# Kernel optimization log

Hardware: AMD Instinct MI355X
Metric: run time of the kernel (lower is better)

The kernel has to match this reference:

```python
import jax, jax.numpy as jnp
import numpy as np

N_NODES = 50000
N_EDGES = 800000
T_STEPS = 12
IN_CH = 2
HID = 64
OUT_CH = 1


def setup_inputs() -> dict:
    key = jax.random.key(0)
    ks = jax.random.split(key, 10)
    x = jax.random.normal(ks[0], (N_NODES, T_STEPS, IN_CH), dtype=jnp.float32)
    edge_index = jax.random.randint(ks[1], (2, N_EDGES), 0, N_NODES, dtype=jnp.int64)
    # GCNConv params (PyG: out = aggregate(norm * (x @ W)) + b)
    W_gcn = jax.random.normal(ks[2], (IN_CH, HID), dtype=jnp.float32) / np.sqrt(IN_CH)
    b_gcn = jnp.zeros((HID,), dtype=jnp.float32)
    # torch.nn.GRU params (1 layer): weight_ih_l0 [3H, H_in], weight_hh_l0 [3H, H]
    s = 1.0 / np.sqrt(HID)
    W_ih = jax.random.uniform(ks[3], (3 * HID, HID), dtype=jnp.float32, minval=-s, maxval=s)
    W_hh = jax.random.uniform(ks[4], (3 * HID, HID), dtype=jnp.float32, minval=-s, maxval=s)
    b_ih = jax.random.uniform(ks[5], (3 * HID,), dtype=jnp.float32, minval=-s, maxval=s)
    b_hh = jax.random.uniform(ks[6], (3 * HID,), dtype=jnp.float32, minval=-s, maxval=s)
    # Linear head
    W_fc = jax.random.uniform(ks[7], (OUT_CH, HID), dtype=jnp.float32, minval=-s, maxval=s)
    b_fc = jax.random.uniform(ks[8], (OUT_CH,), dtype=jnp.float32, minval=-s, maxval=s)
    return {"x": x, "edge_index": edge_index, "W_gcn": W_gcn, "b_gcn": b_gcn,
            "W_ih": W_ih, "W_hh": W_hh, "b_ih": b_ih, "b_hh": b_hh,
            "W_fc": W_fc, "b_fc": b_fc}


def _gcn_norm(edge_index, num_nodes):
    # PyG gcn_norm with self-loops: deg counts incoming edges + self-loop
    src, dst = edge_index[0], edge_index[1]
    deg = jax.ops.segment_sum(jnp.ones_like(dst, dtype=jnp.float32), dst,
                              num_segments=num_nodes) + 1.0  # self-loop
    dinv = jax.lax.rsqrt(deg)
    edge_norm = dinv[src] * dinv[dst]       # [E]
    self_norm = dinv * dinv                 # [N], self-loop weight
    return src, dst, edge_norm, self_norm


def reference(x, edge_index, W_gcn, b_gcn, W_ih, W_hh, b_ih, b_hh, W_fc, b_fc):
    N, T, _ = x.shape
    src, dst, edge_norm, self_norm = _gcn_norm(edge_index, N)

    def gcn(x_t):  # [N, F_in] -> [N, H]
        h = x_t @ W_gcn                                           # [N, H]
        agg = jax.ops.segment_sum(edge_norm[:, None] * h[src], dst,
                                  num_segments=N)                 # gather-scatter
        agg = agg + self_norm[:, None] * h                        # self-loop term
        return jax.nn.relu(agg + b_gcn)

    # small fixed loop over T timesteps (matches original per-timestep GCN)
    spatial = jnp.stack([gcn(x[:, t, :]) for t in range(T)], axis=0)  # [T, N, H]

    H = W_hh.shape[1]
    def gru_step(h, x_t):
        gi = x_t @ W_ih.T + b_ih        # [N, 3H]
        gh = h @ W_hh.T + b_hh          # [N, 3H]
        i_r, i_z, i_n = gi[:, :H], gi[:, H:2 * H], gi[:, 2 * H:]
        h_r, h_z, h_n = gh[:, :H], gh[:, H:2 * H], gh[:, 2 * H:]
        r = jax.nn.sigmoid(i_r + h_r)
        z = jax.nn.sigmoid(i_z + h_z)
        n = jnp.tanh(i_n + r * h_n)
        h_new = (1.0 - z) * n + z * h
        return h_new, None

    h0 = jnp.zeros((N, H), dtype=x.dtype)
    final_rep, _ = jax.lax.scan(gru_step, h0, spatial)  # last hidden state [N, H]
    predictions = final_rep @ W_fc.T + b_fc             # [N, 1]
    return jnp.squeeze(predictions)                     # [N]
```

## Files before the change

### kernel.cpp

```cpp
#include <hip/hip_runtime.h>
#include <hip/hip_fp16.h>
#include <math.h>

#define T_STEPS 12
#define HID 64
#define GWPB 13
#define GBLOCK (GWPB*64)
#define HSTR2 68
#define B_LDS_BYTES 49152
#define WG_LDS_BYTES 1792
#define H_LDS_BYTES (GWPB*16*HSTR2*4)
#define LDS_TOTAL (B_LDS_BYTES + WG_LDS_BYTES + H_LDS_BYTES)

typedef _Float16 half8 __attribute__((ext_vector_type(8)));
typedef __fp16   fp16x2 __attribute__((ext_vector_type(2)));
typedef __attribute__((ext_vector_type(4))) float floatx4;

__device__ __forceinline__ unsigned prm(unsigned a, unsigned b, unsigned s){
  return __builtin_amdgcn_perm(a, b, s);
}
__device__ __forceinline__ float fast_sigmoid(float x){
  float e = __builtin_amdgcn_exp2f(-1.442695041f * x);
  return __builtin_amdgcn_rcpf(1.0f + e);
}
__device__ __forceinline__ float fast_tanh(float x){
  float e = __builtin_amdgcn_exp2f(2.885390082f * x);
  return fmaf(-2.0f, __builtin_amdgcn_rcpf(1.0f + e), 1.0f);
}
__device__ __forceinline__ void split2(float f0, float f1, unsigned &hi, unsigned &lo){
  fp16x2 h = __builtin_amdgcn_cvt_pkrtz(f0, f1);
  float b0 = (float)h[0], b1 = (float)h[1];
  fp16x2 l = __builtin_amdgcn_cvt_pkrtz(f0 - b0, f1 - b1);
  hi = __builtin_bit_cast(unsigned, h);
  lo = __builtin_bit_cast(unsigned, l);
}

__global__ void count_packB_kernel(const int* __restrict__ ei, int E, int* __restrict__ cnt,
                                   int* __restrict__ rank,
                                   const float* __restrict__ W_ih, const float* __restrict__ W_hh,
                                   unsigned short* __restrict__ Bpk){
  int tid = blockIdx.x*blockDim.x + threadIdx.x;
  if (tid < E) rank[tid] = atomicAdd(&cnt[ei[E + tid]], 1);
  if (tid < 48*512){
    int q = tid >> 9;
    int rr = tid & 511;
    int l = rr >> 3, j = rr & 7;
    int g, c4, kt;
    if (q < 32){ g = q >> 4; int rem = q & 15; c4 = rem >> 2; kt = rem & 3; }
    else if (q < 40){ g = 2; c4 = (q-32) >> 1; kt = (q-32) & 1; }
    else            { g = 3; c4 = (q-40) >> 1; kt = ((q-40) & 1) + 2; }
    int k  = kt*32 + (l >> 4)*8 + j;
    int n  = l & 15;
    int jc = c4*16 + n;
    float w;
    if (g == 0)      w = (k < 64) ? W_ih[jc*64 + k]      : W_hh[jc*64 + (k-64)];
    else if (g == 1) w = (k < 64) ? W_ih[(64+jc)*64 + k] : W_hh[(64+jc)*64 + (k-64)];
    else if (g == 2) w = W_ih[(128+jc)*64 + k];
    else             w = W_hh[(128+jc)*64 + (k-64)];
    _Float16 hv = (_Float16)w;
    Bpk[q*512 + l*8 + j] = __builtin_bit_cast(unsigned short, hv);
  }
}

__global__ void dinv_scale_kernel(const int* __restrict__ cnt, const float* __restrict__ x,
                                  float* __restrict__ dinv, float4* __restrict__ xs, int N){
  int tid = blockIdx.x*blockDim.x + threadIdx.x;
  if (tid >= N*6) return;
  int n = tid / 6;
  float dn = rsqrtf((float)cnt[n] + 1.0f);
  if ((tid - n*6) == 0) dinv[n] = dn;
  float4 v = ((const float4*)x)[tid];
  xs[tid] = make_float4(dn*v.x, dn*v.y, dn*v.z, dn*v.w);
}

__global__ void scan1_kernel(const int* __restrict__ cnt, int* __restrict__ part,
                             int* __restrict__ bsum, int N){
  __shared__ int wsum[16];
  int tid = threadIdx.x;
  int g = blockIdx.x*1024 + tid;
  int v = (g < N) ? cnt[g] : 0;
  int lane = tid & 63, wv = tid >> 6;
  int s = v;
  #pragma unroll
  for (int off = 1; off < 64; off <<= 1){
    int u = __shfl_up(s, off, 64);
    if (lane >= off) s += u;
  }
  if (lane == 63) wsum[wv] = s;
  __syncthreads();
  if (wv == 0){
    int w = (lane < 16) ? wsum[lane] : 0;
    #pragma unroll
    for (int off = 1; off < 16; off <<= 1){
      int u = __shfl_up(w, off, 64);
      if (lane >= off) w += u;
    }
    if (lane < 16) wsum[lane] = w;
  }
  __syncthreads();
  int incl = (wv ? wsum[wv-1] : 0) + s;
  if (g < N) part[g] = incl;
  if (tid == 1023) bsum[blockIdx.x] = incl;
}

__global__ void scan3_kernel(const int* __restrict__ part, const int* __restrict__ bsum,
                             const int* __restrict__ cnt, int* __restrict__ row_start,
                             int N, int nb){
  __shared__ int sb[64];
  if (threadIdx.x < 64){
    int v = (threadIdx.x < nb) ? bsum[threadIdx.x] : 0;
    #pragma unroll
    for (int off = 1; off < 64; off <<= 1){
      int u = __shfl_up(v, off, 64);
      if ((int)(threadIdx.x & 63) >= off) v += u;
    }
    sb[threadIdx.x] = v;
  }
  __syncthreads();
  int g = blockIdx.x*blockDim.x + threadIdx.x;
  if (g < N){
    int b = g >> 10;
    int incl = part[g] + (b ? sb[b-1] : 0);
    row_start[g] = incl - cnt[g];
    if (g == N-1) row_start[N] = incl;
  }
}

__global__ void fill_kernel(const int* __restrict__ ei, int E,
                            const int* __restrict__ row_start,
                            const int* __restrict__ rank, int* __restrict__ csr){
  int e = blockIdx.x*blockDim.x + threadIdx.x;
  if (e < E){
    int dst = ei[E + e];
    csr[row_start[dst] + rank[e]] = ei[e];
  }
}

__global__ void gather6_kernel(const float4* __restrict__ xs, const int* __restrict__ row_start,
                               const int* __restrict__ csr, const float* __restrict__ dinv,
                               float4* __restrict__ rin, int N){
  int tid = blockIdx.x*blockDim.x + threadIdx.x;
  if (tid >= N*6) return;
  int n = tid / 6;
  int q = tid - n*6;
  int s0 = row_start[n], s1 = row_start[n+1];
  float4 acc = xs[n*6 + q];
  int e = s0;
  for (; e + 1 < s1; e += 2){
    int sa = csr[e], sb = csr[e+1];
    float4 va = xs[sa*6 + q];
    float4 vb = xs[sb*6 + q];
    acc.x += va.x + vb.x;
    acc.y += va.y + vb.y;
    acc.z += va.z + vb.z;
    acc.w += va.w + vb.w;
  }
  if (e < s1){
    float4 va = xs[csr[e]*6 + q];
    acc.x += va.x; acc.y += va.y; acc.z += va.z; acc.w += va.w;
  }
  float dn = dinv[n];
  rin[tid] = make_float4(dn*acc.x, dn*acc.y, dn*acc.z, dn*acc.w);
}

__global__ __attribute__((amdgpu_waves_per_eu(1, 4))) __launch_bounds__(GBLOCK)
void gru16_kernel(const float* __restrict__ rin,
                  const float* __restrict__ W_gcn, const float* __restrict__ b_gcn,
                  const unsigned short* __restrict__ Bpk,
                  const float* __restrict__ b_ih, const float* __restrict__ b_hh,
                  const float* __restrict__ W_fc, const float* __restrict__ b_fc,
                  float* __restrict__ out, int N, int ntiles){
  extern __shared__ char smem[];
  unsigned short* Bl = (unsigned short*)smem;
  float*    wgl = (float*)(smem + B_LDS_BYTES);
  unsigned* hl  = (unsigned*)(smem + B_LDS_BYTES + WG_LDS_BYTES);

  {
    const int4* Bg = (const int4*)Bpk;
    int4* Bd = (int4*)smem;
    for (int i = threadIdx.x; i < 3072; i += GBLOCK) Bd[i] = Bg[i];
    if (threadIdx.x < 64){
      int l = threadIdx.x;
      wgl[l]       = W_gcn[l];
      wgl[64 + l]  = W_gcn[64 + l];
      wgl[128 + l] = b_gcn[l];
      wgl[192 + 4*l + 0] = b_ih[l]       + b_hh[l];
      wgl[192 + 4*l + 1] = b_ih[64 + l]  + b_hh[64 + l];
      wgl[192 + 4*l + 2] = b_ih[128 + l];
      wgl[192 + 4*l + 3] = b_hh[128 + l];
    }
  }
  __syncthreads();

  int lane = threadIdx.x & 63;
  int wid  = threadIdx.x >> 6;
  int tile = blockIdx.x*GWPB + wid;
  if (tile >= ntiles) return;
  int n0   = tile << 4;
  int quad = lane >> 4;
  int n16  = lane & 15;
  unsigned* hwp = hl + wid*(16*HSTR2);

  for (int i = lane; i < 16*HSTR2; i += 64) hwp[i] = 0u;

  float wfc = W_fc[lane], bfc = b_fc[0];

  int nn = n0 + n16; if (nn > N-1) nn = N-1;
  const float* rbase = rin + (size_t)nn*24;
  float2 rcur = *(const float2*)rbase;

  #pragma unroll 1
  for (int t = 0; t < T_STEPS; ++t){
    float2 rnx = (t < T_STEPS-1) ? *(const float2*)(rbase + 2*(t+1)) : rcur;

    half8 ahi[4], alo[4];
    #pragma unroll
    for (int kt = 0; kt < 2; ++kt){
      int j0 = kt*32 + quad*8;
      floatx4 g0a = *(floatx4*)&wgl[j0],       g0b = *(floatx4*)&wgl[j0+4];
      floatx4 g1a = *(floatx4*)&wgl[64 + j0],  g1b = *(floatx4*)&wgl[64 + j0+4];
      floatx4 bga = *(floatx4*)&wgl[128 + j0], bgb = *(floatx4*)&wgl[128 + j0+4];
      float f[8];
      #pragma unroll
      for (int j = 0; j < 4; ++j){
        f[j]   = fmaxf(fmaf(rcur.x, g0a[j], fmaf(rcur.y, g1a[j], bga[j])), 0.f);
        f[4+j] = fmaxf(fmaf(rcur.x, g0b[j], fmaf(rcur.y, g1b[j], bgb[j])), 0.f);
      }
      union { half8 v; unsigned w[4]; } H, L;
      #pragma unroll
      for (int p2 = 0; p2 < 4; ++p2)
        split2(f[2*p2], f[2*p2+1], H.w[p2], L.w[p2]);
      ahi[kt] = H.v; alo[kt] = L.v;
    }
    #pragma unroll
    for (int kt = 2; kt < 4; ++kt){
      int base = n16*HSTR2 + (kt-2)*32 + quad*8;
      uint4 wa = *(const uint4*)&hwp[base];
      uint4 wb = *(const uint4*)&hwp[base+4];
      union { half8 v; unsigned w[4]; } H, L;
      H.w[0] = prm(wa.y, wa.x, 0x05040100u); L.w[0] = prm(wa.y, wa.x, 0x07060302u);
      H.w[1] = prm(wa.w, wa.z, 0x05040100u); L.w[1] = prm(wa.w, wa.z, 0x07060302u);
      H.w[2] = prm(wb.y, wb.x, 0x05040100u); L.w[2] = prm(wb.y, wb.x, 0x07060302u);
      H.w[3] = prm(wb.w, wb.z, 0x05040100u); L.w[3] = prm(wb.w, wb.z, 0x07060302u);
      ahi[kt] = H.v; alo[kt] = L.v;
    }

    #pragma unroll 2
    for (int c4 = 0; c4 < 4; ++c4){
      int jc = (c4<<4) + n16;
      floatx4 bv = *(floatx4*)&wgl[192 + 4*jc];
      unsigned hpw[4];
      #pragma unroll
      for (int r = 0; r < 4; ++r)
        hpw[r] = hwp[(quad*4 + r)*HSTR2 + (c4<<4) + n16];
      floatx4 aR = (floatx4){bv[0], bv[0], bv[0], bv[0]};
      floatx4 aZ = (floatx4){bv[1], bv[1], bv[1], bv[1]};
      floatx4 aN = (floatx4){bv[2], bv[2], bv[2], bv[2]};
      floatx4 aH = (floatx4){bv[3], bv[3], bv[3], bv[3]};
      #pragma unroll
      for (int kt = 0; kt < 4; ++kt){
        int qr = (c4<<2) + kt;
        half8 wR = *(const half8*)&Bl[qr*512 + lane*8];
        aR = __builtin_amdgcn_mfma_f32_16x16x32_f16(ahi[kt], wR, aR, 0,0,0);
        aR = __builtin_amdgcn_mfma_f32_16x16x32_f16(alo[kt], wR, aR, 0,0,0);
        int qz = 16 + (c4<<2) + kt;
        half8 wZ = *(const half8*)&Bl[qz*512 + lane*8];
        aZ = __builtin_amdgcn_mfma_f32_16x16x32_f16(ahi[kt], wZ, aZ, 0,0,0);
        aZ = __builtin_amdgcn_mfma_f32_16x16x32_f16(alo[kt], wZ, aZ, 0,0,0);
        if (kt < 2){
          int qn = 32 + (c4<<1) + kt;
          half8 wN = *(const half8*)&Bl[qn*512 + lane*8];
          aN = __builtin_amdgcn_mfma_f32_16x16x32_f16(ahi[kt], wN, aN, 0,0,0);
          aN = __builtin_amdgcn_mfma_f32_16x16x32_f16(alo[kt], wN, aN, 0,0,0);
        } else {
          int qh = 40 + (c4<<1) + (kt-2);
          half8 wH = *(const half8*)&Bl[qh*512 + lane*8];
          aH = __builtin_amdgcn_mfma_f32_16x16x32_f16(ahi[kt], wH, aH, 0,0,0);
          aH = __builtin_amdgcn_mfma_f32_16x16x32_f16(alo[kt], wH, aH, 0,0,0);
        }
      }
      #pragma unroll
      for (int r = 0; r < 4; ++r){
        fp16x2 hp2 = __builtin_bit_cast(fp16x2, hpw[r]);
        float hprev = (float)hp2[0] + (float)hp2[1];
        float rg = fast_sigmoid(aR[r]);
        float zg = fast_sigmoid(aZ[r]);
        float ng = fast_tanh(fmaf(rg, aH[r], aN[r]));
        float hn = fmaf(zg, hprev - ng, ng);
        fp16x2 t0 = __builtin_amdgcn_cvt_pkrtz(hn, hn);
        float back = (float)t0[0];
        fp16x2 pw = __builtin_amdgcn_cvt_pkrtz(hn, hn - back);
        hwp[(quad*4 + r)*HSTR2 + (c4<<4) + n16] = __builtin_bit_cast(unsigned, pw);
      }
    }
    rcur = rnx;
  }

  #pragma unroll 1
  for (int m = 0; m < 16; ++m){
    fp16x2 hw2 = __builtin_bit_cast(fp16x2, hwp[m*HSTR2 + lane]);
    float hv = (float)hw2[0] + (float)hw2[1];
    float v = hv * wfc;
    #pragma unroll
    for (int off = 32; off >= 1; off >>= 1) v += __shfl_xor(v, off, 64);
    int n = n0 + m;
    if (lane == 0 && n < N) out[n] = v + bfc;
  }
}

extern "C" void kernel_launch(void* const* d_in, const int* in_sizes, int n_in,
                              void* d_out, int out_size, void* d_ws, size_t ws_size,
                              hipStream_t stream){
  const float* x     = (const float*)d_in[0];
  const int*   ei    = (const int*)d_in[1];
  const float* W_gcn = (const float*)d_in[2];
  const float* b_gcn = (const float*)d_in[3];
  const float* W_ih  = (const float*)d_in[4];
  const float* W_hh  = (const float*)d_in[5];
  const float* b_ih  = (const float*)d_in[6];
  const float* b_hh  = (const float*)d_in[7];
  const float* W_fc  = (const float*)d_in[8];
  const float* b_fc  = (const float*)d_in[9];
  float* out = (float*)d_out;
  const int N = in_sizes[0] / (T_STEPS*2);
  const int E = in_sizes[1] / 2;
  const int NB1024 = (N + 1023) / 1024;

  char* p = (char*)d_ws;
  auto alloc = [&](size_t bytes)->char*{
    char* r = p; p += (bytes + 255) & ~(size_t)255; return r;
  };
  int*   cnt       = (int*)  alloc((size_t)N*4);
  int*   row_start = (int*)  alloc((size_t)(N+1)*4);
  int*   rank      = (int*)  alloc((size_t)E*4);
  int*   csr       = (int*)  alloc((size_t)E*4);
  float* dinv      = (float*)alloc((size_t)N*4);
  int*   part      = (int*)  alloc((size_t)N*4);
  int*   bsum      = (int*)  alloc((size_t)NB1024*4);
  float* rin       = (float*)alloc((size_t)N*24*4);
  float* xs        = (float*)alloc((size_t)N*24*4);
  unsigned short* Bpk = (unsigned short*)alloc((size_t)24576*2);

  hipMemsetAsync(cnt, 0, (size_t)N*4, stream);
  {
    int work = (E > 48*512) ? E : 48*512;
    count_packB_kernel<<<(work+255)/256, 256, 0, stream>>>(ei, E, cnt, rank, W_ih, W_hh, Bpk);
  }
  dinv_scale_kernel<<<(N*6+255)/256, 256, 0, stream>>>(cnt, x, dinv, (float4*)xs, N);
  scan1_kernel<<<NB1024, 1024, 0, stream>>>(cnt, part, bsum, N);
  scan3_kernel<<<(N+255)/256, 256, 0, stream>>>(part, bsum, cnt, row_start, N, NB1024);
  fill_kernel<<<(E+255)/256, 256, 0, stream>>>(ei, E, row_start, rank, csr);
  gather6_kernel<<<(N*6+255)/256, 256, 0, stream>>>((const float4*)xs, row_start, csr,
                                                    dinv, (float4*)rin, N);

  (void)hipFuncSetAttribute((const void*)gru16_kernel,
                            hipFuncAttributeMaxDynamicSharedMemorySize, LDS_TOTAL);
  int ntiles = (N + 15) / 16;
  int blocks = (ntiles + GWPB - 1) / GWPB;
  gru16_kernel<<<blocks, GBLOCK, LDS_TOTAL, stream>>>(rin, W_gcn, b_gcn, Bpk,
                                                      b_ih, b_hh, W_fc, b_fc,
                                                      out, N, ntiles);
}
```

Measured before the change: 237.5 us.

## Process two 16-node subtiles per wave in GRU kernel to reuse weight loads

Each wave now handles 32 nodes (two 16-row MFMA tiles) instead of 16, so every B-weight fragment read from LDS feeds two MFMA chains. Waves per block drop from 13 to 7 and the waves-per-EU hint is lowered to allow more registers. This halves LDS weight traffic per node and gives the scheduler two independent MFMA dependency chains to interleave, at the cost of higher register pressure, lower occupancy and fewer waves to hide latency.

Result: slower. 247.1 us (+4.0%).

```diff
diff --git a/kernel.cpp b/kernel.cpp
--- a/kernel.cpp
+++ b/kernel.cpp
@@ -4,12 +4,12 @@
 
 #define T_STEPS 12
 #define HID 64
-#define GWPB 13
+#define GWPB 7
 #define GBLOCK (GWPB*64)
 #define HSTR2 68
 #define B_LDS_BYTES 49152
 #define WG_LDS_BYTES 1792
-#define H_LDS_BYTES (GWPB*16*HSTR2*4)
+#define H_LDS_BYTES (GWPB*32*HSTR2*4)
 #define LDS_TOTAL (B_LDS_BYTES + WG_LDS_BYTES + H_LDS_BYTES)
 
 typedef _Float16 half8 __attribute__((ext_vector_type(8)));
@@ -163,7 +163,7 @@
   rin[tid] = make_float4(dn*acc.x, dn*acc.y, dn*acc.z, dn*acc.w);
 }
 
-__global__ __attribute__((amdgpu_waves_per_eu(1, 4))) __launch_bounds__(GBLOCK)
+__global__ __attribute__((amdgpu_waves_per_eu(1, 2))) __launch_bounds__(GBLOCK)
 void gru16_kernel(const float* __restrict__ rin,
                   const float* __restrict__ W_gcn, const float* __restrict__ b_gcn,
                   const unsigned short* __restrict__ Bpk,
@@ -196,108 +196,148 @@
   int wid  = threadIdx.x >> 6;
   int tile = blockIdx.x*GWPB + wid;
   if (tile >= ntiles) return;
-  int n0   = tile << 4;
+  int n0   = tile << 5;
   int quad = lane >> 4;
   int n16  = lane & 15;
-  unsigned* hwp = hl + wid*(16*HSTR2);
-
-  for (int i = lane; i < 16*HSTR2; i += 64) hwp[i] = 0u;
+  unsigned* hwp = hl + wid*(32*HSTR2);
+
+  for (int i = lane; i < 32*HSTR2; i += 64) hwp[i] = 0u;
 
   float wfc = W_fc[lane], bfc = b_fc[0];
 
-  int nn = n0 + n16; if (nn > N-1) nn = N-1;
-  const float* rbase = rin + (size_t)nn*24;
-  float2 rcur = *(const float2*)rbase;
+  int nn  = n0 + n16;      if (nn  > N-1) nn  = N-1;
+  int nn2 = n0 + 16 + n16; if (nn2 > N-1) nn2 = N-1;
+  const float* rbase  = rin + (size_t)nn*24;
+  const float* rbase2 = rin + (size_t)nn2*24;
+  float2 rcur  = *(const float2*)rbase;
+  float2 rcur2 = *(const float2*)rbase2;
 
   #pragma unroll 1
   for (int t = 0; t < T_STEPS; ++t){
-    float2 rnx = (t < T_STEPS-1) ? *(const float2*)(rbase + 2*(t+1)) : rcur;
-
-    half8 ahi[4], alo[4];
+    float2 rnx  = (t < T_STEPS-1) ? *(const float2*)(rbase  + 2*(t+1)) : rcur;
+    float2 rnx2 = (t < T_STEPS-1) ? *(const float2*)(rbase2 + 2*(t+1)) : rcur2;
+
+    half8 ahi0[4], alo0[4], ahi1[4], alo1[4];
     #pragma unroll
     for (int kt = 0; kt < 2; ++kt){
       int j0 = kt*32 + quad*8;
       floatx4 g0a = *(floatx4*)&wgl[j0],       g0b = *(floatx4*)&wgl[j0+4];
       floatx4 g1a = *(floatx4*)&wgl[64 + j0],  g1b = *(floatx4*)&wgl[64 + j0+4];
       floatx4 bga = *(floatx4*)&wgl[128 + j0], bgb = *(floatx4*)&wgl[128 + j0+4];
-      float f[8];
+      float f0[8], f1[8];
       #pragma unroll
       for (int j = 0; j < 4; ++j){
-        f[j]   = fmaxf(fmaf(rcur.x, g0a[j], fmaf(rcur.y, g1a[j], bga[j])), 0.f);
-        f[4+j] = fmaxf(fmaf(rcur.x, g0b[j], fmaf(rcur.y, g1b[j], bgb[j])), 0.f);
-      }
-      union { half8 v; unsigned w[4]; } H, L;
-      #pragma unroll
-      for (int p2 = 0; p2 < 4; ++p2)
-        split2(f[2*p2], f[2*p2+1], H.w[p2], L.w[p2]);
-      ahi[kt] = H.v; alo[kt] = L.v;
+        f0[j]   = fmaxf(fmaf(rcur.x,  g0a[j], fmaf(rcur.y,  g1a[j], bga[j])), 0.f);
+        f0[4+j] = fmaxf(fmaf(rcur.x,  g0b[j], fmaf(rcur.y,  g1b[j], bgb[j])), 0.f);
+        f1[j]   = fmaxf(fmaf(rcur2.x, g0a[j], fmaf(rcur2.y, g1a[j], bga[j])), 0.f);
+        f1[4+j] = fmaxf(fmaf(rcur2.x, g0b[j], fmaf(rcur2.y, g1b[j], bgb[j])), 0.f);
+      }
+      union { half8 v; unsigned w[4]; } H0, L0, H1, L1;
+      #pragma unroll
+      for (int p2 = 0; p2 < 4; ++p2){
+        split2(f0[2*p2], f0[2*p2+1], H0.w[p2], L0.w[p2]);
+        split2(f1[2*p2], f1[2*p2+1], H1.w[p2], L1.w[p2]);
+      }
+      ahi0[kt] = H0.v; alo0[kt] = L0.v;
+      ahi1[kt] = H1.v; alo1[kt] = L1.v;
     }
     #pragma unroll
     for (int kt = 2; kt < 4; ++kt){
-      int base = n16*HSTR2 + (kt-2)*32 + quad*8;
-      uint4 wa = *(const uint4*)&hwp[base];
-      uint4 wb = *(const uint4*)&hwp[base+4];
-      union { half8 v; unsigned w[4]; } H, L;
-      H.w[0] = prm(wa.y, wa.x, 0x05040100u); L.w[0] = prm(wa.y, wa.x, 0x07060302u);
-      H.w[1] = prm(wa.w, wa.z, 0x05040100u); L.w[1] = prm(wa.w, wa.z, 0x07060302u);
-      H.w[2] = prm(wb.y, wb.x, 0x05040100u); L.w[2] = prm(wb.y, wb.x, 0x07060302u);
-      H.w[3] = prm(wb.w, wb.z, 0x05040100u); L.w[3] = prm(wb.w, wb.z, 0x07060302u);
-      ahi[kt] = H.v; alo[kt] = L.v;
+      int base0 = n16*HSTR2       + (kt-2)*32 + quad*8;
+      int base1 = (16+n16)*HSTR2  + (kt-2)*32 + quad*8;
+      uint4 wa = *(const uint4*)&hwp[base0];
+      uint4 wb = *(const uint4*)&hwp[base0+4];
+      uint4 wc = *(const uint4*)&hwp[base1];
+      uint4 wd = *(const uint4*)&hwp[base1+4];
+      union { half8 v; unsigned w[4]; } H0, L0, H1, L1;
+      H0.w[0] = prm(wa.y, wa.x, 0x05040100u); L0.w[0] = prm(wa.y, wa.x, 0x07060302u);
+      H0.w[1] = prm(wa.w, wa.z, 0x05040100u); L0.w[1] = prm(wa.w, wa.z, 0x07060302u);
+      H0.w[2] = prm(wb.y, wb.x, 0x05040100u); L0.w[2] = prm(wb.y, wb.x, 0x07060302u);
+      H0.w[3] = prm(wb.w, wb.z, 0x05040100u); L0.w[3] = prm(wb.w, wb.z, 0x07060302u);
+      H1.w[0] = prm(wc.y, wc.x, 0x05040100u); L1.w[0] = prm(wc.y, wc.x, 0x07060302u);
+      H1.w[1] = prm(wc.w, wc.z, 0x05040100u); L1.w[1] = prm(wc.w, wc.z, 0x07060302u);
+      H1.w[2] = prm(wd.y, wd.x, 0x05040100u); L1.w[2] = prm(wd.y, wd.x, 0x07060302u);
+      H1.w[3] = prm(wd.w, wd.z, 0x05040100u); L1.w[3] = prm(wd.w, wd.z, 0x07060302u);
+      ahi0[kt] = H0.v; alo0[kt] = L0.v;
+      ahi1[kt] = H1.v; alo1[kt] = L1.v;
     }
 
     #pragma unroll 2
     for (int c4 = 0; c4 < 4; ++c4){
       int jc = (c4<<4) + n16;
       floatx4 bv = *(floatx4*)&wgl[192 + 4*jc];
-      unsigned hpw[4];
-      #pragma unroll
-      for (int r = 0; r < 4; ++r)
-        hpw[r] = hwp[(quad*4 + r)*HSTR2 + (c4<<4) + n16];
-      floatx4 aR = (floatx4){bv[0], bv[0], bv[0], bv[0]};
-      floatx4 aZ = (floatx4){bv[1], bv[1], bv[1], bv[1]};
-      floatx4 aN = (floatx4){bv[2], bv[2], bv[2], bv[2]};
-      floatx4 aH = (floatx4){bv[3], bv[3], bv[3], bv[3]};
+      unsigned hpw0[4], hpw1[4];
+      #pragma unroll
+      for (int r = 0; r < 4; ++r){
+        hpw0[r] = hwp[(quad*4 + r)*HSTR2      + (c4<<4) + n16];
+        hpw1[r] = hwp[(16 + quad*4 + r)*HSTR2 + (c4<<4) + n16];
+      }
+      floatx4 aR0 = (floatx4){bv[0], bv[0], bv[0], bv[0]}, aR1 = aR0;
+      floatx4 aZ0 = (floatx4){bv[1], bv[1], bv[1], bv[1]}, aZ1 = aZ0;
+      floatx4 aN0 = (floatx4){bv[2], bv[2], bv[2], bv[2]}, aN1 = aN0;
+      floatx4 aH0 = (floatx4){bv[3], bv[3], bv[3], bv[3]}, aH1 = aH0;
       #pragma unroll
       for (int kt = 0; kt < 4; ++kt){
         int qr = (c4<<2) + kt;
         half8 wR = *(const half8*)&Bl[qr*512 + lane*8];
-        aR = __builtin_amdgcn_mfma_f32_16x16x32_f16(ahi[kt], wR, aR, 0,0,0);
-        aR = __builtin_amdgcn_mfma_f32_16x16x32_f16(alo[kt], wR, aR, 0,0,0);
+        aR0 = __builtin_amdgcn_mfma_f32_16x16x32_f16(ahi0[kt], wR, aR0, 0,0,0);
+        aR0 = __builtin_amdgcn_mfma_f32_16x16x32_f16(alo0[kt], wR, aR0, 0,0,0);
+        aR1 = __builtin_amdgcn_mfma_f32_16x16x32_f16(ahi1[kt], wR, aR1, 0,0,0);
+        aR1 = __builtin_amdgcn_mfma_f32_16x16x32_f16(alo1[kt], wR, aR1, 0,0,0);
         int qz = 16 + (c4<<2) + kt;
         half8 wZ = *(const half8*)&Bl[qz*512 + lane*8];
-        aZ = __builtin_amdgcn_mfma_f32_16x16x32_f16(ahi[kt], wZ, aZ, 0,0,0);
-        aZ = __builtin_amdgcn_mfma_f32_16x16x32_f16(alo[kt], wZ, aZ, 0,0,0);
+        aZ0 = __builtin_amdgcn_mfma_f32_16x16x32_f16(ahi0[kt], wZ, aZ0, 0,0,0);
+        aZ0 = __builtin_amdgcn_mfma_f32_16x16x32_f16(alo0[kt], wZ, aZ0, 0,0,0);
+        aZ1 = __builtin_amdgcn_mfma_f32_16x16x32_f16(ahi1[kt], wZ, aZ1, 0,0,0);
+        aZ1 = __builtin_amdgcn_mfma_f32_16x16x32_f16(alo1[kt], wZ, aZ1, 0,0,0);
         if (kt < 2){
           int qn = 32 + (c4<<1) + kt;
           half8 wN = *(const half8*)&Bl[qn*512 + lane*8];
-          aN = __builtin_amdgcn_mfma_f32_16x16x32_f16(ahi[kt], wN, aN, 0,0,0);
-          aN = __builtin_amdgcn_mfma_f32_16x16x32_f16(alo[kt], wN, aN, 0,0,0);
+          aN0 = __builtin_amdgcn_mfma_f32_16x16x32_f16(ahi0[kt], wN, aN0, 0,0,0);
+          aN0 = __builtin_amdgcn_mfma_f32_16x16x32_f16(alo0[kt], wN, aN0, 0,0,0);
+          aN1 = __builtin_amdgcn_mfma_f32_16x16x32_f16(ahi1[kt], wN, aN1, 0,0,0);
+          aN1 = __builtin_amdgcn_mfma_f32_16x16x32_f16(alo1[kt], wN, aN1, 0,0,0);
         } else {
           int qh = 40 + (c4<<1) + (kt-2);
           half8 wH = *(const half8*)&Bl[qh*512 + lane*8];
-          aH = __builtin_amdgcn_mfma_f32_16x16x32_f16(ahi[kt], wH, aH, 0,0,0);
-          aH = __builtin_amdgcn_mfma_f32_16x16x32_f16(alo[kt], wH, aH, 0,0,0);
+          aH0 = __builtin_amdgcn_mfma_f32_16x16x32_f16(ahi0[kt], wH, aH0, 0,0,0);
+          aH0 = __builtin_amdgcn_mfma_f32_16x16x32_f16(alo0[kt], wH, aH0, 0,0,0);
+          aH1 = __builtin_amdgcn_mfma_f32_16x16x32_f16(ahi1[kt], wH, aH1, 0,0,0);
+          aH1 = __builtin_amdgcn_mfma_f32_16x16x32_f16(alo1[kt], wH, aH1, 0,0,0);
         }
       }
       #pragma unroll
       for (int r = 0; r < 4; ++r){
-        fp16x2 hp2 = __builtin_bit_cast(fp16x2, hpw[r]);
+        fp16x2 hp2 = __builtin_bit_cast(fp16x2, hpw0[r]);
         float hprev = (float)hp2[0] + (float)hp2[1];
-        float rg = fast_sigmoid(aR[r]);
-        float zg = fast_sigmoid(aZ[r]);
-        float ng = fast_tanh(fmaf(rg, aH[r], aN[r]));
+        float rg = fast_sigmoid(aR0[r]);
+        float zg = fast_sigmoid(aZ0[r]);
+        float ng = fast_tanh(fmaf(rg, aH0[r], aN0[r]));
         float hn = fmaf(zg, hprev - ng, ng);
         fp16x2 t0 = __builtin_amdgcn_cvt_pkrtz(hn, hn);
         float back = (float)t0[0];
         fp16x2 pw = __builtin_amdgcn_cvt_pkrtz(hn, hn - back);
         hwp[(quad*4 + r)*HSTR2 + (c4<<4) + n16] = __builtin_bit_cast(unsigned, pw);
       }
-    }
-    rcur = rnx;
+      #pragma unroll
+      for (int r = 0; r < 4; ++r){
+        fp16x2 hp2 = __builtin_bit_cast(fp16x2, hpw1[r]);
+        float hprev = (float)hp2[0] + (float)hp2[1];
+        float rg = fast_sigmoid(aR1[r]);
+        float zg = fast_sigmoid(aZ1[r]);
+        float ng = fast_tanh(fmaf(rg, aH1[r], aN1[r]));
+        float hn = fmaf(zg, hprev - ng, ng);
+        fp16x2 t0 = __builtin_amdgcn_cvt_pkrtz(hn, hn);
+        float back = (float)t0[0];
+        fp16x2 pw = __builtin_amdgcn_cvt_pkrtz(hn, hn - back);
+        hwp[(16 + quad*4 + r)*HSTR2 + (c4<<4) + n16] = __builtin_bit_cast(unsigned, pw);
+      }
+    }
+    rcur = rnx; rcur2 = rnx2;
   }
 
   #pragma unroll 1
-  for (int m = 0; m < 16; ++m){
+  for (int m = 0; m < 32; ++m){
     fp16x2 hw2 = __builtin_bit_cast(fp16x2, hwp[m*HSTR2 + lane]);
     float hv = (float)hw2[0] + (float)hw2[1];
     float v = hv * wfc;
@@ -355,7 +395,7 @@
 
   (void)hipFuncSetAttribute((const void*)gru16_kernel,
                             hipFuncAttributeMaxDynamicSharedMemorySize, LDS_TOTAL);
-  int ntiles = (N + 15) / 16;
+  int ntiles = (N + 31) / 32;
   int blocks = (ntiles + GWPB - 1) / GWPB;
   gru16_kernel<<<blocks, GBLOCK, LDS_TOTAL, stream>>>(rin, W_gcn, b_gcn, Bpk,
                                                       b_ih, b_hh, W_fc, b_fc,
```
